# Optimization experiments

Measured on AMD Instinct MI355X. Metric: run time of the kernel, lower is better.

Reference implementation:

```python
import jax, jax.numpy as jnp
import numpy as np
from functools import partial

WS = 11          # window size (safe for H=W=256)
SIGMA = 1.5
DATA_RANGE = 1.0
EPS = 1e-8


def _gaussian_window(ws: int, sigma: float, channels: int) -> jnp.ndarray:
    coords = jnp.arange(ws, dtype=jnp.float32) - ws // 2
    g = jnp.exp(-(coords ** 2) / (2.0 * sigma * sigma))
    g = g / (g.sum() + 1e-12)
    win2d = jnp.outer(g, g)                      # [ws, ws]
    # depthwise kernel: OIHW with O=C, I=1, feature_group_count=C
    return jnp.broadcast_to(win2d, (channels, 1, ws, ws))


def _depthwise_conv(x: jnp.ndarray, win: jnp.ndarray) -> jnp.ndarray:
    # x: [N, C, H, W]; same-padding depthwise Gaussian filter
    c = x.shape[1]
    pad = WS // 2
    return jax.lax.conv_general_dilated(
        x, win,
        window_strides=(1, 1),
        padding=[(pad, pad), (pad, pad)],
        dimension_numbers=('NCHW', 'OIHW', 'NCHW'),
        feature_group_count=c,
    )


def setup_inputs() -> dict:
    key = jax.random.key(0)
    k1, k2 = jax.random.split(key)
    shape = (8, 8, 3, 256, 256)  # [B, T, C, H, W]
    pred = jax.random.uniform(k1, shape, dtype=jnp.float32)
    target = jax.random.uniform(k2, shape, dtype=jnp.float32)
    return {"pred": pred, "target": target}


def reference(pred, target):
    pred = jnp.clip(pred.astype(jnp.float32), 0.0, 1.0)
    target = jnp.clip(target.astype(jnp.float32), 0.0, 1.0)
    B, T, C, H, W = pred.shape
    x = pred.reshape(B * T, C, H, W)
    y = target.reshape(B * T, C, H, W)

    win = _gaussian_window(WS, SIGMA, C)

    mu_x = _depthwise_conv(x, win)
    mu_y = _depthwise_conv(y, win)
    mu_x2 = mu_x * mu_x
    mu_y2 = mu_y * mu_y
    mu_xy = mu_x * mu_y

    sigma_x2 = jnp.maximum(_depthwise_conv(x * x, win) - mu_x2, 0.0)
    sigma_y2 = jnp.maximum(_depthwise_conv(y * y, win) - mu_y2, 0.0)
    sigma_xy = _depthwise_conv(x * y, win) - mu_xy

    C1 = (0.01 * DATA_RANGE) ** 2
    C2 = (0.03 * DATA_RANGE) ** 2
    num = (2.0 * mu_xy + C1) * (2.0 * sigma_xy + C2)
    den = (mu_x2 + mu_y2 + C1) * (sigma_x2 + sigma_y2 + C2)
    ssim_map = num / (den + EPS)
    ssim_map = jnp.nan_to_num(ssim_map, nan=0.0, posinf=0.0, neginf=0.0)
    return 1.0 - jnp.mean(ssim_map)
```

## Files before the change

### kernel.cpp

```cpp
#include <hip/hip_runtime.h>


typedef _Float16 h2 __attribute__((ext_vector_type(2)));
typedef __fp16 fp16v2 __attribute__((ext_vector_type(2)));

#define WSZ 11
#define RAD 5
#define IMH 256
#define IMW 256
#define BAND 4
#define NBANDS (IMH / BAND)
#define NPLANES 192
#define NWAVETOT (NPLANES * NBANDS)
#define WPB 4
#define NGRID (NWAVETOT / WPB)
#define NPIXF (192.0f * 256.0f * 256.0f)

#define GW0 0.001028381f
#define GW1 0.007598770f
#define GW2 0.036000770f
#define GW3 0.109360600f
#define GW4 0.213005700f
#define GW5 0.266011790f

__device__ __forceinline__ h2 pk_fma16(h2 a, h2 b, h2 c) {
    h2 d;
    asm("v_pk_fma_f16 %0, %1, %2, %3" : "=v"(d) : "v"(a), "v"(b), "v"(c));
    return d;
}
__device__ __forceinline__ h2 pk_mul16(h2 a, h2 b) {
    h2 d;
    asm("v_pk_mul_f16 %0, %1, %2" : "=v"(d) : "v"(a), "v"(b));
    return d;
}
__device__ __forceinline__ h2 pk_add16(h2 a, h2 b) {
    h2 d;
    asm("v_pk_add_f16 %0, %1, %2" : "=v"(d) : "v"(a), "v"(b));
    return d;
}

union H2U { h2 h; unsigned u; };
__device__ __forceinline__ unsigned h2u(h2 v) { H2U x; x.h = v; return x.u; }
__device__ __forceinline__ h2 u2h(unsigned v) { H2U x; x.u = v; return x.h; }

__device__ __forceinline__ h2 bperm(int idx, h2 v) {
    return u2h((unsigned)__builtin_amdgcn_ds_bpermute(idx, (int)h2u(v)));
}
__device__ __forceinline__ h2 albt(h2 hi, h2 lo) {
    return u2h(__builtin_amdgcn_alignbit(h2u(hi), h2u(lo), 16));
}

__device__ __forceinline__ h2 splat16(float s) {
    _Float16 t = (_Float16)s;
    return (h2){t, t};
}
__device__ __forceinline__ h2 zero16() { return (h2){(_Float16)0, (_Float16)0}; }

__device__ __forceinline__ h2 clip_pack(float a, float b) {
    a = fminf(fmaxf(a, 0.f), 1.f);
    b = fminf(fmaxf(b, 0.f), 1.f);
    fp16v2 r = __builtin_amdgcn_cvt_pkrtz(a, b);
    return __builtin_bit_cast(h2, r);
}

__global__ __launch_bounds__(256, 4) void ssim_band_kernel(
    const float* __restrict__ pred,
    const float* __restrict__ targ,
    float* __restrict__ partial)
{
    const int tid = threadIdx.x;
    const int lane = tid & 63;
    const int wid = tid >> 6;
    const int b = blockIdx.x * WPB + wid;
    const int plane = b >> 6;
    const int band = b & 63;
    const int r0 = band * BAND;

    const float4* __restrict__ pp =
        (const float4*)(pred + (size_t)plane * (IMH * IMW));
    const float4* __restrict__ tp =
        (const float4*)(targ + (size_t)plane * (IMH * IMW));

    const h2 W0 = splat16(GW0), W1 = splat16(GW1), W2 = splat16(GW2),
             W3 = splat16(GW3), W4 = splat16(GW4), W5 = splat16(GW5);
    const h2 wv16[WSZ] = {W0, W1, W2, W3, W4, W5, W4, W3, W2, W1, W0};
    const h2 M2 = splat16(-2.0f);

    const int iu1 = (lane - 1) << 2;
    const int iu2 = (lane - 2) << 2;
    const int id1 = (lane + 1) << 2;
    const int id2 = (lane + 2) << 2;
    const bool mu1 = lane >= 1;
    const bool mu2 = lane >= 2;
    const bool md1 = lane <= 62;
    const bool md2 = lane <= 61;

    h2 RS[WSZ][2], RD[WSZ][2];

#pragma unroll
    for (int j = 0; j < 10; ++j) {
        const int r = r0 - RAD + j;
        const int rc = min(max(r, 0), IMH - 1);
        const bool oob = (r < 0) | (r >= IMH);
        const float4 a = pp[rc * 64 + lane];
        const float4 c = tp[rc * 64 + lane];
        const h2 x0 = clip_pack(a.x, a.y), x1 = clip_pack(a.z, a.w);
        const h2 y0 = clip_pack(c.x, c.y), y1 = clip_pack(c.z, c.w);
        h2 s0 = pk_add16(x0, y0);
        h2 s1 = pk_add16(x1, y1);
        h2 d0 = pk_fma16(M2, y0, s0);
        h2 d1 = pk_fma16(M2, y1, s1);
        RS[j][0] = oob ? zero16() : s0;
        RS[j][1] = oob ? zero16() : s1;
        RD[j][0] = oob ? zero16() : d0;
        RD[j][1] = oob ? zero16() : d1;
    }

    float4 PA[2], PC[2];
    {
        const int ra = min(r0 + RAD, IMH - 1);
        const int rb = min(r0 + RAD + 1, IMH - 1);
        PA[0] = pp[ra * 64 + lane]; PC[0] = tp[ra * 64 + lane];
        PA[1] = pp[rb * 64 + lane]; PC[1] = tp[rb * 64 + lane];
    }

    const float C1 = 1e-4f, C2 = 9e-4f;
    float lsum = 0.f;

#pragma unroll
    for (int i = 0; i < BAND; ++i) {
        const int sIn = (i + 10) % WSZ;
        {
            const float4 a = PA[i & 1], c = PC[i & 1];
            const bool oob = (r0 + RAD + i) >= IMH;
            const h2 x0 = clip_pack(a.x, a.y), x1 = clip_pack(a.z, a.w);
            const h2 y0 = clip_pack(c.x, c.y), y1 = clip_pack(c.z, c.w);
            h2 s0 = pk_add16(x0, y0);
            h2 s1 = pk_add16(x1, y1);
            h2 d0 = pk_fma16(M2, y0, s0);
            h2 d1 = pk_fma16(M2, y1, s1);
            RS[sIn][0] = oob ? zero16() : s0;
            RS[sIn][1] = oob ? zero16() : s1;
            RD[sIn][0] = oob ? zero16() : d0;
            RD[sIn][1] = oob ? zero16() : d1;
        }

        {
            const int rn = min(r0 + RAD + i + 2, IMH - 1);
            PA[i & 1] = pp[rn * 64 + lane];
            PC[i & 1] = tp[rn * 64 + lane];
        }

        h2 vd[4][2];
#pragma unroll
        for (int p = 0; p < 2; ++p) {
            vd[0][p] = zero16(); vd[1][p] = zero16();
            vd[2][p] = zero16(); vd[3][p] = zero16();
        }
#pragma unroll
        for (int k = 0; k < WSZ; ++k) {
            const int sl = (i + k) % WSZ;
            const h2 wk = wv16[k];
#pragma unroll
            for (int p = 0; p < 2; ++p) {
                const h2 s = RS[sl][p], d = RD[sl][p];
                const h2 ws = pk_mul16(wk, s);
                const h2 wd = pk_mul16(wk, d);
                vd[0][p] = pk_add16(vd[0][p], ws);
                vd[1][p] = pk_add16(vd[1][p], wd);
                vd[2][p] = pk_fma16(ws, s, vd[2][p]);
                vd[3][p] = pk_fma16(wd, d, vd[3][p]);
            }
        }

        h2 hf[4][2];
#pragma unroll
        for (int ch = 0; ch < 4; ++ch) {
            const h2 H0 = vd[ch][0], H1 = vd[ch][1];
            h2 Gm3 = bperm(iu2, H1);
            h2 Gm2 = bperm(iu1, H0);
            h2 Gm1 = bperm(iu1, H1);
            h2 G2  = bperm(id1, H0);
            h2 G3  = bperm(id1, H1);
            h2 G4  = bperm(id2, H0);
            Gm3 = mu2 ? Gm3 : zero16();
            Gm2 = mu1 ? Gm2 : zero16();
            Gm1 = mu1 ? Gm1 : zero16();
            G2  = md1 ? G2  : zero16();
            G3  = md1 ? G3  : zero16();
            G4  = md2 ? G4  : zero16();
            const h2 P0  = albt(Gm2, Gm3);
            const h2 P1  = Gm2;
            const h2 P2  = albt(Gm1, Gm2);
            const h2 P3  = Gm1;
            const h2 P4  = albt(H0, Gm1);
            const h2 P5  = H0;
            const h2 P6  = albt(H1, H0);
            const h2 P7  = H1;
            const h2 P8  = albt(G2, H1);
            const h2 P9  = G2;
            const h2 P10 = albt(G3, G2);
            const h2 P11 = G3;
            const h2 P12 = albt(G4, G3);
            h2 a0 = pk_mul16(W0, P0);
            a0 = pk_fma16(W1, P1, a0);
            a0 = pk_fma16(W2, P2, a0);
            a0 = pk_fma16(W3, P3, a0);
            a0 = pk_fma16(W4, P4, a0);
            a0 = pk_fma16(W5, P5, a0);
            a0 = pk_fma16(W4, P6, a0);
            a0 = pk_fma16(W3, P7, a0);
            a0 = pk_fma16(W2, P8, a0);
            a0 = pk_fma16(W1, P9, a0);
            a0 = pk_fma16(W0, P10, a0);
            h2 a1 = pk_mul16(W0, P2);
            a1 = pk_fma16(W1, P3, a1);
            a1 = pk_fma16(W2, P4, a1);
            a1 = pk_fma16(W3, P5, a1);
            a1 = pk_fma16(W4, P6, a1);
            a1 = pk_fma16(W5, P7, a1);
            a1 = pk_fma16(W4, P8, a1);
            a1 = pk_fma16(W3, P9, a1);
            a1 = pk_fma16(W2, P10, a1);
            a1 = pk_fma16(W1, P11, a1);
            a1 = pk_fma16(W0, P12, a1);
            hf[ch][0] = a0;
            hf[ch][1] = a1;
        }

#pragma unroll
        for (int p = 0; p < 2; ++p) {
#pragma unroll
            for (int e = 0; e < 2; ++e) {
                const float ms = (float)hf[0][p][e];
                const float md = (float)hf[1][p][e];
                const float Ss = (float)hf[2][p][e];
                const float Sd = (float)hf[3][p][e];
                const float P = ms * ms, Q = md * md;
                const float mxy2 = 0.5f * (P - Q);
                const float m2s  = 0.5f * (P + Q);
                const float Ssum = 0.5f * (Ss + Sd);
                const float ssum = fmaxf(Ssum - m2s, 0.f);
                const float sxy2 = fmaf(0.5f, Ss - Sd, -mxy2);
                const float num = (mxy2 + C1) * (sxy2 + C2);
                const float den = fmaf(m2s + C1, ssum + C2, 1e-8f);
                lsum += num * __builtin_amdgcn_rcpf(den);
            }
        }
    }

#pragma unroll
    for (int off = 32; off > 0; off >>= 1)
        lsum += __shfl_xor(lsum, off, 64);

    __shared__ float wsum[WPB];
    if (lane == 0) wsum[wid] = lsum;
    __syncthreads();
    if (tid == 0)
        partial[blockIdx.x] = wsum[0] + wsum[1] + wsum[2] + wsum[3];
}

__global__ __launch_bounds__(256) void ssim_finalize(
    const float* __restrict__ partial,
    float* __restrict__ out)
{
    __shared__ float wsum[4];
    const int t = threadIdx.x;
    float s = 0.f;
    for (int i = t; i < NGRID; i += 256) s += partial[i];
#pragma unroll
    for (int off = 32; off > 0; off >>= 1)
        s += __shfl_xor(s, off, 64);
    const int lane = t & 63, wv = t >> 6;
    if (lane == 0) wsum[wv] = s;
    __syncthreads();
    if (t == 0)
        out[0] = 1.0f - (wsum[0] + wsum[1] + wsum[2] + wsum[3]) / NPIXF;
}

extern "C" void kernel_launch(void* const* d_in, const int* in_sizes, int n_in,
                              void* d_out, int out_size, void* d_ws, size_t ws_size,
                              hipStream_t stream) {
    const float* pred = (const float*)d_in[0];
    const float* targ = (const float*)d_in[1];
    float* out = (float*)d_out;
    float* part = (float*)d_ws;

    ssim_band_kernel<<<NGRID, 256, 0, stream>>>(pred, targ, part);
    ssim_finalize<<<1, 256, 0, stream>>>(part, out);
}
```

Measured before the change: 140.5 us.

## Share halo rows across block waves via LDS instead of per-wave register windows

Each block now covers a 16-row band. Its four waves cooperatively load the 26 halo rows once, convert them to packed fp16 sum/diff values and store them in LDS. Each wave then runs the vertical filter on 4 rows by reading from LDS, instead of reloading 14 rows per 4-row band from global memory. This cuts redundant global reads and conversion work from halo overlap, at the cost of LDS traffic, a block barrier and less load/compute overlap. The clamp is also moved to packed fp16 min/max after conversion.

Measured after the change: 142.5 us. No clear change (+1.4%).

```diff
diff --git a/kernel.cpp b/kernel.cpp
--- a/kernel.cpp
+++ b/kernel.cpp
@@ -8,12 +8,13 @@
 #define RAD 5
 #define IMH 256
 #define IMW 256
-#define BAND 4
-#define NBANDS (IMH / BAND)
+#define BROWS 16
+#define HROWS (BROWS + 2 * RAD)
+#define NBANDS (IMH / BROWS)
 #define NPLANES 192
-#define NWAVETOT (NPLANES * NBANDS)
+#define NGRID (NPLANES * NBANDS)
 #define WPB 4
-#define NGRID (NWAVETOT / WPB)
+#define RPW (BROWS / WPB)
 #define NPIXF (192.0f * 256.0f * 256.0f)
 
 #define GW0 0.001028381f
@@ -38,6 +39,16 @@
     asm("v_pk_add_f16 %0, %1, %2" : "=v"(d) : "v"(a), "v"(b));
     return d;
 }
+__device__ __forceinline__ h2 pk_min16(h2 a, h2 b) {
+    h2 d;
+    asm("v_pk_min_f16 %0, %1, %2" : "=v"(d) : "v"(a), "v"(b));
+    return d;
+}
+__device__ __forceinline__ h2 pk_max16(h2 a, h2 b) {
+    h2 d;
+    asm("v_pk_max_f16 %0, %1, %2" : "=v"(d) : "v"(a), "v"(b));
+    return d;
+}
 
 union H2U { h2 h; unsigned u; };
 __device__ __forceinline__ unsigned h2u(h2 v) { H2U x; x.h = v; return x.u; }
@@ -56,11 +67,10 @@
 }
 __device__ __forceinline__ h2 zero16() { return (h2){(_Float16)0, (_Float16)0}; }
 
-__device__ __forceinline__ h2 clip_pack(float a, float b) {
-    a = fminf(fmaxf(a, 0.f), 1.f);
-    b = fminf(fmaxf(b, 0.f), 1.f);
+__device__ __forceinline__ h2 clip_pack(float a, float b, h2 Z, h2 O) {
     fp16v2 r = __builtin_amdgcn_cvt_pkrtz(a, b);
-    return __builtin_bit_cast(h2, r);
+    h2 v = __builtin_bit_cast(h2, r);
+    return pk_min16(pk_max16(v, Z), O);
 }
 
 __global__ __launch_bounds__(256, 4) void ssim_band_kernel(
@@ -71,10 +81,10 @@
     const int tid = threadIdx.x;
     const int lane = tid & 63;
     const int wid = tid >> 6;
-    const int b = blockIdx.x * WPB + wid;
-    const int plane = b >> 6;
-    const int band = b & 63;
-    const int r0 = band * BAND;
+    const int blk = blockIdx.x;
+    const int plane = blk >> 4;
+    const int band = blk & 15;
+    const int r0 = band * BROWS;
 
     const float4* __restrict__ pp =
         (const float4*)(pred + (size_t)plane * (IMH * IMW));
@@ -85,6 +95,34 @@
              W3 = splat16(GW3), W4 = splat16(GW4), W5 = splat16(GW5);
     const h2 wv16[WSZ] = {W0, W1, W2, W3, W4, W5, W4, W3, W2, W1, W0};
     const h2 M2 = splat16(-2.0f);
+    const h2 Z16 = zero16();
+    const h2 O16 = splat16(1.0f);
+
+    __shared__ uint4 lds[HROWS * 64];
+    __shared__ float wsum[WPB];
+
+    for (int j = wid; j < HROWS; j += WPB) {
+        const int r = r0 - RAD + j;
+        const int rc = min(max(r, 0), IMH - 1);
+        const bool oob = (r < 0) | (r >= IMH);
+        const float4 a = pp[rc * 64 + lane];
+        const float4 c = tp[rc * 64 + lane];
+        const h2 x0 = clip_pack(a.x, a.y, Z16, O16);
+        const h2 x1 = clip_pack(a.z, a.w, Z16, O16);
+        const h2 y0 = clip_pack(c.x, c.y, Z16, O16);
+        const h2 y1 = clip_pack(c.z, c.w, Z16, O16);
+        const h2 s0 = pk_add16(x0, y0);
+        const h2 s1 = pk_add16(x1, y1);
+        const h2 d0 = pk_fma16(M2, y0, s0);
+        const h2 d1 = pk_fma16(M2, y1, s1);
+        uint4 w;
+        w.x = oob ? 0u : h2u(s0);
+        w.y = oob ? 0u : h2u(d0);
+        w.z = oob ? 0u : h2u(s1);
+        w.w = oob ? 0u : h2u(d1);
+        lds[j * 64 + lane] = w;
+    }
+    __syncthreads();
 
     const int iu1 = (lane - 1) << 2;
     const int iu2 = (lane - 2) << 2;
@@ -95,61 +133,12 @@
     const bool md1 = lane <= 62;
     const bool md2 = lane <= 61;
 
-    h2 RS[WSZ][2], RD[WSZ][2];
-
-#pragma unroll
-    for (int j = 0; j < 10; ++j) {
-        const int r = r0 - RAD + j;
-        const int rc = min(max(r, 0), IMH - 1);
-        const bool oob = (r < 0) | (r >= IMH);
-        const float4 a = pp[rc * 64 + lane];
-        const float4 c = tp[rc * 64 + lane];
-        const h2 x0 = clip_pack(a.x, a.y), x1 = clip_pack(a.z, a.w);
-        const h2 y0 = clip_pack(c.x, c.y), y1 = clip_pack(c.z, c.w);
-        h2 s0 = pk_add16(x0, y0);
-        h2 s1 = pk_add16(x1, y1);
-        h2 d0 = pk_fma16(M2, y0, s0);
-        h2 d1 = pk_fma16(M2, y1, s1);
-        RS[j][0] = oob ? zero16() : s0;
-        RS[j][1] = oob ? zero16() : s1;
-        RD[j][0] = oob ? zero16() : d0;
-        RD[j][1] = oob ? zero16() : d1;
-    }
-
-    float4 PA[2], PC[2];
-    {
-        const int ra = min(r0 + RAD, IMH - 1);
-        const int rb = min(r0 + RAD + 1, IMH - 1);
-        PA[0] = pp[ra * 64 + lane]; PC[0] = tp[ra * 64 + lane];
-        PA[1] = pp[rb * 64 + lane]; PC[1] = tp[rb * 64 + lane];
-    }
-
     const float C1 = 1e-4f, C2 = 9e-4f;
     float lsum = 0.f;
 
 #pragma unroll
-    for (int i = 0; i < BAND; ++i) {
-        const int sIn = (i + 10) % WSZ;
-        {
-            const float4 a = PA[i & 1], c = PC[i & 1];
-            const bool oob = (r0 + RAD + i) >= IMH;
-            const h2 x0 = clip_pack(a.x, a.y), x1 = clip_pack(a.z, a.w);
-            const h2 y0 = clip_pack(c.x, c.y), y1 = clip_pack(c.z, c.w);
-            h2 s0 = pk_add16(x0, y0);
-            h2 s1 = pk_add16(x1, y1);
-            h2 d0 = pk_fma16(M2, y0, s0);
-            h2 d1 = pk_fma16(M2, y1, s1);
-            RS[sIn][0] = oob ? zero16() : s0;
-            RS[sIn][1] = oob ? zero16() : s1;
-            RD[sIn][0] = oob ? zero16() : d0;
-            RD[sIn][1] = oob ? zero16() : d1;
-        }
-
-        {
-            const int rn = min(r0 + RAD + i + 2, IMH - 1);
-            PA[i & 1] = pp[rn * 64 + lane];
-            PC[i & 1] = tp[rn * 64 + lane];
-        }
+    for (int i = 0; i < RPW; ++i) {
+        const int jb = wid * RPW + i;
 
         h2 vd[4][2];
 #pragma unroll
@@ -159,18 +148,22 @@
         }
 #pragma unroll
         for (int k = 0; k < WSZ; ++k) {
-            const int sl = (i + k) % WSZ;
+            const uint4 v = lds[(jb + k) * 64 + lane];
             const h2 wk = wv16[k];
-#pragma unroll
-            for (int p = 0; p < 2; ++p) {
-                const h2 s = RS[sl][p], d = RD[sl][p];
-                const h2 ws = pk_mul16(wk, s);
-                const h2 wd = pk_mul16(wk, d);
-                vd[0][p] = pk_add16(vd[0][p], ws);
-                vd[1][p] = pk_add16(vd[1][p], wd);
-                vd[2][p] = pk_fma16(ws, s, vd[2][p]);
-                vd[3][p] = pk_fma16(wd, d, vd[3][p]);
-            }
+            const h2 sA = u2h(v.x), dA = u2h(v.y);
+            const h2 sB = u2h(v.z), dB = u2h(v.w);
+            h2 ws = pk_mul16(wk, sA);
+            h2 wd = pk_mul16(wk, dA);
+            vd[0][0] = pk_add16(vd[0][0], ws);
+            vd[1][0] = pk_add16(vd[1][0], wd);
+            vd[2][0] = pk_fma16(ws, sA, vd[2][0]);
+            vd[3][0] = pk_fma16(wd, dA, vd[3][0]);
+            ws = pk_mul16(wk, sB);
+            wd = pk_mul16(wk, dB);
+            vd[0][1] = pk_add16(vd[0][1], ws);
+            vd[1][1] = pk_add16(vd[1][1], wd);
+            vd[2][1] = pk_fma16(ws, sB, vd[2][1]);
+            vd[3][1] = pk_fma16(wd, dB, vd[3][1]);
         }
 
         h2 hf[4][2];
@@ -253,11 +246,10 @@
     for (int off = 32; off > 0; off >>= 1)
         lsum += __shfl_xor(lsum, off, 64);
 
-    __shared__ float wsum[WPB];
     if (lane == 0) wsum[wid] = lsum;
     __syncthreads();
     if (tid == 0)
-        partial[blockIdx.x] = wsum[0] + wsum[1] + wsum[2] + wsum[3];
+        partial[blk] = wsum[0] + wsum[1] + wsum[2] + wsum[3];
 }
 
 __global__ __launch_bounds__(256) void ssim_finalize(
```
